# Kernel optimization log

Hardware: AMD Instinct MI355X
Metric: run time of the kernel (lower is better)

Reference implementation:

```python
import jax, jax.numpy as jnp
import numpy as np

N_NODES = 100000
N_EDGES = 1600000
D_IN = 128
LAYER_SIZES = [128, 128, 64]


def setup_inputs() -> dict:
    key = jax.random.key(0)
    ks = jax.random.split(key, 12)
    x = jax.random.normal(ks[0], (N_NODES, D_IN), dtype=jnp.float32)
    edge_index = jax.random.randint(ks[1], (2, N_EDGES), 0, N_NODES, dtype=jnp.int64)
    edge_weight = jax.random.uniform(ks[2], (N_EDGES,), dtype=jnp.float32)
    inp = {"x": x, "edge_index": edge_index, "edge_weight": edge_weight}
    dims = [D_IN] + LAYER_SIZES
    for i in range(len(LAYER_SIZES)):
        fan_in, fan_out = dims[i], dims[i + 1]
        # glorot-style init like PyG GCNConv
        scale = jnp.sqrt(6.0 / (fan_in + fan_out)).astype(jnp.float32)
        inp[f"W{i}"] = jax.random.uniform(ks[3 + 2 * i], (fan_in, fan_out), dtype=jnp.float32, minval=-scale, maxval=scale)
        inp[f"b{i}"] = jnp.zeros((fan_out,), dtype=jnp.float32)
    return inp


def _gcn_norm(edge_index, edge_weight, num_nodes):
    # PyG gcn_norm with add_self_loops=True (fill value 1.0)
    src, dst = edge_index[0], edge_index[1]
    loop = jnp.arange(num_nodes, dtype=edge_index.dtype)
    src_full = jnp.concatenate([src, loop])
    dst_full = jnp.concatenate([dst, loop])
    w_full = jnp.concatenate([edge_weight, jnp.ones((num_nodes,), dtype=edge_weight.dtype)])
    deg = jax.ops.segment_sum(w_full, dst_full, num_segments=num_nodes)  # [N]
    deg_inv_sqrt = jnp.where(deg > 0, jax.lax.rsqrt(jnp.where(deg > 0, deg, 1.0)), 0.0)
    norm = deg_inv_sqrt[src_full] * w_full * deg_inv_sqrt[dst_full]  # [E+N]
    return src_full, dst_full, norm


def _gcn_conv(x, src, dst, norm, W, b):
    h = x @ W                                  # [N, d_out] dense transform
    msg = h[src] * norm[:, None]               # [E+N, d_out] gather + scale
    out = jax.ops.segment_sum(msg, dst, num_segments=x.shape[0])  # scatter-add
    return out + b


def reference(x, edge_index, edge_weight, W0, b0, W1, b1, W2, b2):
    N = x.shape[0]
    src, dst, norm = _gcn_norm(edge_index, edge_weight, N)
    x = jax.nn.relu(_gcn_conv(x, src, dst, norm, W0, b0))
    x = jax.nn.relu(_gcn_conv(x, src, dst, norm, W1, b1))
    x = _gcn_conv(x, src, dst, norm, W2, b2)  # no ReLU on final layer
    return x
```

## Files before the change

kernel.cpp:

```cpp
#include <hip/hip_runtime.h>
#include <hip/hip_fp16.h>


typedef __attribute__((ext_vector_type(8))) _Float16 f16x8;
typedef __attribute__((ext_vector_type(4))) float f32x4;

#define WQ_BITS 15
#define WQ_SCALE 32768.0f
#define WQ_MASK 32767u

__global__ __launch_bounds__(256) void k_init(int* cnt, int N) {
    int i = blockIdx.x * 256 + threadIdx.x;
    if (i < N) cnt[i] = 0;
}

__global__ __launch_bounds__(256) void k_wprep(const float* __restrict__ W0,
                                               const float* __restrict__ W1,
                                               const float* __restrict__ W2,
                                               __half* __restrict__ wt0,
                                               __half* __restrict__ wt1,
                                               __half* __restrict__ wt2) {
    int id = blockIdx.x * 256 + threadIdx.x;
    if (id < 16384) {
        int n = id >> 7, k = id & 127;
        wt0[id] = __float2half(W0[k * 128 + n]);
    } else if (id < 32768) {
        int j = id - 16384, n = j >> 7, k = j & 127;
        wt1[j] = __float2half(W1[k * 128 + n]);
    } else if (id < 40960) {
        int j = id - 32768, n = j >> 7, k = j & 127;
        wt2[j] = __float2half(W2[k * 64 + n]);
    }
}

__global__ __launch_bounds__(256) void k_build(const int* __restrict__ src,
                                               const int* __restrict__ dst,
                                               const float* __restrict__ w,
                                               int* cnt, unsigned int* __restrict__ EW,
                                               int E, int cap) {
    int e = blockIdx.x * 256 + threadIdx.x;
    if (e >= E) return;
    int s = src[e], t = dst[e];
    int wq = (int)(w[e] * WQ_SCALE + 0.5f);
    wq = (wq < (int)WQ_MASK) ? wq : (int)WQ_MASK;
    int k = atomicAdd(&cnt[t], 1);
    if (k < cap) EW[(size_t)t * cap + k] = ((unsigned int)s << WQ_BITS) | (unsigned int)wq;
}

__global__ __launch_bounds__(256) void k_dinv(const int* __restrict__ cnt,
                                              const unsigned int* __restrict__ EW,
                                              float* __restrict__ dinv, int N, int cap) {
    int node = blockIdx.x * 4 + (threadIdx.x >> 6);
    if (node >= N) return;
    int lane = threadIdx.x & 63;
    int c = cnt[node];
    c = (c < cap) ? c : cap;
    float w = 0.f;
    if (lane < c) w = (float)(EW[(size_t)node * cap + lane] & WQ_MASK);
#pragma unroll
    for (int o = 32; o > 0; o >>= 1) w += __shfl_xor(w, o, 64);
    if (lane == 0) {
        float deg = 1.0f + w * (1.0f / WQ_SCALE);
        dinv[node] = 1.0f / sqrtf(deg);
    }
}

template <int BN, bool XFP32>
__global__ __launch_bounds__(256, 4) void k_gemm(const void* __restrict__ Xv,
                                                 const __half* __restrict__ Wt,
                                                 const float* __restrict__ dinv,
                                                 __half* __restrict__ H, int N) {
    constexpr int NT = BN / 16;
    const int lane = threadIdx.x & 63;
    const int wv = threadIdx.x >> 6;
    const int m = lane & 15;
    const int quad = lane >> 4;
    const int row = blockIdx.x * 64 + wv * 16 + m;
    const int rowc = (row < N) ? row : (N - 1);

    f16x8 xf[4];
    if constexpr (XFP32) {
        const float* X = (const float*)Xv;
#pragma unroll
        for (int s = 0; s < 4; s++) {
            const float4* p = (const float4*)(X + (size_t)rowc * 128 + s * 32 + quad * 8);
            float4 u0 = p[0], u1 = p[1];
            f16x8 f;
            f[0] = (_Float16)u0.x; f[1] = (_Float16)u0.y;
            f[2] = (_Float16)u0.z; f[3] = (_Float16)u0.w;
            f[4] = (_Float16)u1.x; f[5] = (_Float16)u1.y;
            f[6] = (_Float16)u1.z; f[7] = (_Float16)u1.w;
            xf[s] = f;
        }
    } else {
        const __half* X = (const __half*)Xv;
#pragma unroll
        for (int s = 0; s < 4; s++)
            xf[s] = *(const f16x8*)(X + (size_t)rowc * 128 + s * 32 + quad * 8);
    }

    f32x4 acc[NT];
#pragma unroll
    for (int t = 0; t < NT; t++) acc[t] = (f32x4){0.f, 0.f, 0.f, 0.f};

#pragma unroll
    for (int s = 0; s < 4; s++) {
#pragma unroll
        for (int t = 0; t < NT; t++) {
            f16x8 wf = *(const f16x8*)(Wt + (size_t)(t * 16 + m) * 128 + s * 32 + quad * 8);
            acc[t] = __builtin_amdgcn_mfma_f32_16x16x32_f16(wf, xf[s], acc[t], 0, 0, 0);
        }
    }

    if (row < N) {
        float sc = dinv[row];
#pragma unroll
        for (int t = 0; t < NT; t++) {
            __half2 h0 = __floats2half2_rn(sc * acc[t][0], sc * acc[t][1]);
            __half2 h1 = __floats2half2_rn(sc * acc[t][2], sc * acc[t][3]);
            __half2* dstp = (__half2*)(H + (size_t)row * BN + t * 16 + quad * 4);
            dstp[0] = h0;
            dstp[1] = h1;
        }
    }
}

#define RL(v, k) __builtin_amdgcn_readlane((v), (k))

template <int DOUT, bool RELU>
__global__ __launch_bounds__(256) void k_agg(const __half* __restrict__ H,
                                             const unsigned int* __restrict__ EW,
                                             const int* __restrict__ cnt,
                                             const float* __restrict__ dinv,
                                             const float* __restrict__ bias,
                                             void* __restrict__ Outv,
                                             int N, int cap) {
    int node = blockIdx.x * 4 + (threadIdx.x >> 6);
    if (node >= N) return;
    const int lane = threadIdx.x & 63;

    int c = cnt[node];
    c = (c < cap) ? c : cap;

    unsigned int meta = 0;
    if (lane < c) meta = EW[(size_t)node * cap + lane];

    float dt = dinv[node];

    if constexpr (DOUT == 128) {
        const __half2* H2 = reinterpret_cast<const __half2*>(H);
        float2 hs = __half22float2(H2[(size_t)node * 64 + lane]);
        float a0 = hs.x, a1 = hs.y;
        int k = 0;
        for (; k + 8 <= c; k += 8) {
            __half2 hr[8]; float w[8];
#pragma unroll
            for (int u = 0; u < 8; u++) {
                unsigned int mm = RL(meta, k + u);
                w[u] = (float)(mm & WQ_MASK) * (1.0f / WQ_SCALE);
                hr[u] = H2[(size_t)(mm >> WQ_BITS) * 64 + lane];
            }
#pragma unroll
            for (int u = 0; u < 8; u++) {
                float2 hv = __half22float2(hr[u]);
                a0 = fmaf(w[u], hv.x, a0);
                a1 = fmaf(w[u], hv.y, a1);
            }
        }
        for (; k + 4 <= c; k += 4) {
            __half2 hr[4]; float w[4];
#pragma unroll
            for (int u = 0; u < 4; u++) {
                unsigned int mm = RL(meta, k + u);
                w[u] = (float)(mm & WQ_MASK) * (1.0f / WQ_SCALE);
                hr[u] = H2[(size_t)(mm >> WQ_BITS) * 64 + lane];
            }
#pragma unroll
            for (int u = 0; u < 4; u++) {
                float2 hv = __half22float2(hr[u]);
                a0 = fmaf(w[u], hv.x, a0);
                a1 = fmaf(w[u], hv.y, a1);
            }
        }
        for (; k < c; k++) {
            unsigned int mm = RL(meta, k);
            float w = (float)(mm & WQ_MASK) * (1.0f / WQ_SCALE);
            float2 hv = __half22float2(H2[(size_t)(mm >> WQ_BITS) * 64 + lane]);
            a0 = fmaf(w, hv.x, a0);
            a1 = fmaf(w, hv.y, a1);
        }
        float2 b = reinterpret_cast<const float2*>(bias)[lane];
        a0 = fmaf(dt, a0, b.x);
        a1 = fmaf(dt, a1, b.y);
        if (RELU) { a0 = fmaxf(a0, 0.f); a1 = fmaxf(a1, 0.f); }
        reinterpret_cast<__half2*>(Outv)[(size_t)node * 64 + lane] = __floats2half2_rn(a0, a1);
    } else {
        float a = __half2float(H[(size_t)node * 64 + lane]);
        int k = 0;
        for (; k + 8 <= c; k += 8) {
            __half hr[8]; float w[8];
#pragma unroll
            for (int u = 0; u < 8; u++) {
                unsigned int mm = RL(meta, k + u);
                w[u] = (float)(mm & WQ_MASK) * (1.0f / WQ_SCALE);
                hr[u] = H[(size_t)(mm >> WQ_BITS) * 64 + lane];
            }
#pragma unroll
            for (int u = 0; u < 8; u++) a = fmaf(w[u], __half2float(hr[u]), a);
        }
        for (; k < c; k++) {
            unsigned int mm = RL(meta, k);
            float w = (float)(mm & WQ_MASK) * (1.0f / WQ_SCALE);
            a = fmaf(w, __half2float(H[(size_t)(mm >> WQ_BITS) * 64 + lane]), a);
        }
        a = fmaf(dt, a, bias[lane]);
        if (RELU) a = fmaxf(a, 0.f);
        ((float*)Outv)[(size_t)node * 64 + lane] = a;
    }
}

extern "C" void kernel_launch(void* const* d_in, const int* in_sizes, int n_in,
                              void* d_out, int out_size, void* d_ws, size_t ws_size,
                              hipStream_t stream) {
    const int N = in_sizes[0] / 128;
    const int E = in_sizes[2];

    const float* x  = (const float*)d_in[0];
    const int*   ei = (const int*)d_in[1];
    const int*   src = ei;
    const int*   dst = ei + E;
    const float* ew  = (const float*)d_in[2];
    const float* W0 = (const float*)d_in[3];
    const float* b0 = (const float*)d_in[4];
    const float* W1 = (const float*)d_in[5];
    const float* b1 = (const float*)d_in[6];
    const float* W2 = (const float*)d_in[7];
    const float* b2 = (const float*)d_in[8];

    size_t fixed = (((size_t)N * 4 + 255) & ~(size_t)255)
                 + (((size_t)N * 4 + 255) & ~(size_t)255)
                 + 2 * (((size_t)N * 128 * 2 + 255) & ~(size_t)255)
                 + 3 * 33024
                 + 2048;
    int cap = 64;
    if (ws_size > fixed) {
        size_t avail = (ws_size - fixed) / ((size_t)N * 4);
        if (avail < (size_t)cap) cap = (int)avail;
    } else {
        cap = 0;
    }

    char* p = (char*)d_ws;
    auto alloc = [&](size_t bytes) -> void* {
        void* r = (void*)p;
        p += (bytes + 255) & ~(size_t)255;
        return r;
    };
    int*          cnt  = (int*)alloc((size_t)N * 4);
    float*        dinv = (float*)alloc((size_t)N * 4);
    unsigned int* EW   = (unsigned int*)alloc((size_t)N * cap * 4);
    __half*       bufH = (__half*)alloc((size_t)N * 128 * 2);
    __half*       bufA = (__half*)alloc((size_t)N * 128 * 2);
    __half*       wt0  = (__half*)alloc(16384 * 2);
    __half*       wt1  = (__half*)alloc(16384 * 2);
    __half*       wt2  = (__half*)alloc(8192 * 2);

    dim3 blk(256);
    dim3 gN((N + 255) / 256), gE((E + 255) / 256);
    dim3 gGemm((N + 63) / 64);
    dim3 gWave((N + 3) / 4);

    k_init<<<gN, blk, 0, stream>>>(cnt, N);
    k_wprep<<<160, blk, 0, stream>>>(W0, W1, W2, wt0, wt1, wt2);
    k_build<<<gE, blk, 0, stream>>>(src, dst, ew, cnt, EW, E, cap);
    k_dinv<<<gWave, blk, 0, stream>>>(cnt, EW, dinv, N, cap);

    k_gemm<128, true><<<gGemm, blk, 0, stream>>>(x, wt0, dinv, bufH, N);
    k_agg<128, true><<<gWave, blk, 0, stream>>>(bufH, EW, cnt, dinv, b0, bufA, N, cap);

    k_gemm<128, false><<<gGemm, blk, 0, stream>>>(bufA, wt1, dinv, bufH, N);
    k_agg<128, true><<<gWave, blk, 0, stream>>>(bufH, EW, cnt, dinv, b1, bufA, N, cap);

    k_gemm<64, false><<<gGemm, blk, 0, stream>>>(bufA, wt2, dinv, bufH, N);
    k_agg<64, false><<<gWave, blk, 0, stream>>>(bufH, EW, cnt, dinv, b2,
                                                d_out, N, cap);
}
```

Baseline: 483.7 us.

## Fuse init/wprep, partition build atomics by dst group, fold dinv into first GEMM

Merges the counter-zeroing and weight-prep kernels into one launch, and folds the degree/dinv computation into the first GEMM kernel, which now computes dinv per block into shared memory and also writes it out. The edge-build kernel now uses a fixed grid where each block handles only edges whose destination falls in one of 8 partitions (by (t>>4)&7). The goal is to localize atomic traffic and CSR writes per partition, likely for better cache/XCD locality. In exchange, every edge is read 8 times for the filter check, and the GEMM gains a serial per-row degree loop before its MFMA work.

Result: faster. 448.2 us (-7.4%).

```diff
diff --git a/kernel.cpp b/kernel.cpp
--- a/kernel.cpp
+++ b/kernel.cpp
@@ -9,18 +9,15 @@
 #define WQ_SCALE 32768.0f
 #define WQ_MASK 32767u
 
-__global__ __launch_bounds__(256) void k_init(int* cnt, int N) {
-    int i = blockIdx.x * 256 + threadIdx.x;
-    if (i < N) cnt[i] = 0;
-}
-
-__global__ __launch_bounds__(256) void k_wprep(const float* __restrict__ W0,
-                                               const float* __restrict__ W1,
-                                               const float* __restrict__ W2,
-                                               __half* __restrict__ wt0,
-                                               __half* __restrict__ wt1,
-                                               __half* __restrict__ wt2) {
+__global__ __launch_bounds__(256) void k_pre(int* cnt, int N,
+                                             const float* __restrict__ W0,
+                                             const float* __restrict__ W1,
+                                             const float* __restrict__ W2,
+                                             __half* __restrict__ wt0,
+                                             __half* __restrict__ wt1,
+                                             __half* __restrict__ wt2) {
     int id = blockIdx.x * 256 + threadIdx.x;
+    if (id < N) cnt[id] = 0;
     if (id < 16384) {
         int n = id >> 7, k = id & 127;
         wt0[id] = __float2half(W0[k * 128 + n]);
@@ -38,45 +35,58 @@
                                                const float* __restrict__ w,
                                                int* cnt, unsigned int* __restrict__ EW,
                                                int E, int cap) {
-    int e = blockIdx.x * 256 + threadIdx.x;
-    if (e >= E) return;
-    int s = src[e], t = dst[e];
-    int wq = (int)(w[e] * WQ_SCALE + 0.5f);
-    wq = (wq < (int)WQ_MASK) ? wq : (int)WQ_MASK;
-    int k = atomicAdd(&cnt[t], 1);
-    if (k < cap) EW[(size_t)t * cap + k] = ((unsigned int)s << WQ_BITS) | (unsigned int)wq;
-}
-
-__global__ __launch_bounds__(256) void k_dinv(const int* __restrict__ cnt,
-                                              const unsigned int* __restrict__ EW,
-                                              float* __restrict__ dinv, int N, int cap) {
-    int node = blockIdx.x * 4 + (threadIdx.x >> 6);
-    if (node >= N) return;
-    int lane = threadIdx.x & 63;
-    int c = cnt[node];
-    c = (c < cap) ? c : cap;
-    float w = 0.f;
-    if (lane < c) w = (float)(EW[(size_t)node * cap + lane] & WQ_MASK);
-#pragma unroll
-    for (int o = 32; o > 0; o >>= 1) w += __shfl_xor(w, o, 64);
-    if (lane == 0) {
-        float deg = 1.0f + w * (1.0f / WQ_SCALE);
-        dinv[node] = 1.0f / sqrtf(deg);
-    }
-}
-
-template <int BN, bool XFP32>
+    const int p = blockIdx.x & 7;
+    const int chunk = blockIdx.x >> 3;
+    const int nchunk = gridDim.x >> 3;
+    const int stride = nchunk * 256;
+    for (int e = chunk * 256 + threadIdx.x; e < E; e += stride) {
+        int t = dst[e];
+        if (((t >> 4) & 7) != p) continue;
+        int s = src[e];
+        int wq = (int)(w[e] * WQ_SCALE + 0.5f);
+        wq = (wq < (int)WQ_MASK) ? wq : (int)WQ_MASK;
+        int k = atomicAdd(&cnt[t], 1);
+        if (k < cap) EW[(size_t)t * cap + k] = ((unsigned int)s << WQ_BITS) | (unsigned int)wq;
+    }
+}
+
+template <int BN, bool XFP32, bool DINV>
 __global__ __launch_bounds__(256, 4) void k_gemm(const void* __restrict__ Xv,
                                                  const __half* __restrict__ Wt,
-                                                 const float* __restrict__ dinv,
+                                                 float* __restrict__ dinv,
+                                                 const int* __restrict__ cnt,
+                                                 const unsigned int* __restrict__ EW,
+                                                 int cap,
                                                  __half* __restrict__ H, int N) {
-    constexpr int NT = BN / 16;
-    const int lane = threadIdx.x & 63;
-    const int wv = threadIdx.x >> 6;
+    __shared__ float dinv_s[64];
+    const int tid = threadIdx.x;
+    const int lane = tid & 63;
+    const int wv = tid >> 6;
     const int m = lane & 15;
     const int quad = lane >> 4;
-    const int row = blockIdx.x * 64 + wv * 16 + m;
+    const int rb = blockIdx.x * 64;
+    const int row = rb + wv * 16 + m;
     const int rowc = (row < N) ? row : (N - 1);
+
+    if constexpr (DINV) {
+        int rloc = tid >> 2, sub = tid & 3;
+        int r = rb + rloc;
+        float wsum = 0.f;
+        if (r < N) {
+            int c = cnt[r];
+            c = (c < cap) ? c : cap;
+            for (int j = sub; j < c; j += 4)
+                wsum += (float)(EW[(size_t)r * cap + j] & WQ_MASK);
+        }
+        wsum += __shfl_xor(wsum, 1, 64);
+        wsum += __shfl_xor(wsum, 2, 64);
+        float dv = 1.0f / sqrtf(1.0f + wsum * (1.0f / WQ_SCALE));
+        if (sub == 0) {
+            dinv_s[rloc] = dv;
+            if (r < N) dinv[r] = dv;
+        }
+        __syncthreads();
+    }
 
     f16x8 xf[4];
     if constexpr (XFP32) {
@@ -99,6 +109,7 @@
             xf[s] = *(const f16x8*)(X + (size_t)rowc * 128 + s * 32 + quad * 8);
     }
 
+    constexpr int NT = BN / 16;
     f32x4 acc[NT];
 #pragma unroll
     for (int t = 0; t < NT; t++) acc[t] = (f32x4){0.f, 0.f, 0.f, 0.f};
@@ -113,7 +124,7 @@
     }
 
     if (row < N) {
-        float sc = dinv[row];
+        float sc = DINV ? dinv_s[wv * 16 + m] : dinv[row];
 #pragma unroll
         for (int t = 0; t < NT; t++) {
             __half2 h0 = __floats2half2_rn(sc * acc[t][0], sc * acc[t][1]);
@@ -266,22 +277,22 @@
     __half*       wt2  = (__half*)alloc(8192 * 2);
 
     dim3 blk(256);
-    dim3 gN((N + 255) / 256), gE((E + 255) / 256);
+    int preN = (N > 40960) ? N : 40960;
+    dim3 gPre((preN + 255) / 256);
+    dim3 gBuild(6656);
     dim3 gGemm((N + 63) / 64);
     dim3 gWave((N + 3) / 4);
 
-    k_init<<<gN, blk, 0, stream>>>(cnt, N);
-    k_wprep<<<160, blk, 0, stream>>>(W0, W1, W2, wt0, wt1, wt2);
-    k_build<<<gE, blk, 0, stream>>>(src, dst, ew, cnt, EW, E, cap);
-    k_dinv<<<gWave, blk, 0, stream>>>(cnt, EW, dinv, N, cap);
-
-    k_gemm<128, true><<<gGemm, blk, 0, stream>>>(x, wt0, dinv, bufH, N);
+    k_pre<<<gPre, blk, 0, stream>>>(cnt, N, W0, W1, W2, wt0, wt1, wt2);
+    k_build<<<gBuild, blk, 0, stream>>>(src, dst, ew, cnt, EW, E, cap);
+
+    k_gemm<128, true, true><<<gGemm, blk, 0, stream>>>(x, wt0, dinv, cnt, EW, cap, bufH, N);
     k_agg<128, true><<<gWave, blk, 0, stream>>>(bufH, EW, cnt, dinv, b0, bufA, N, cap);
 
-    k_gemm<128, false><<<gGemm, blk, 0, stream>>>(bufA, wt1, dinv, bufH, N);
+    k_gemm<128, false, false><<<gGemm, blk, 0, stream>>>(bufA, wt1, dinv, cnt, EW, cap, bufH, N);
     k_agg<128, true><<<gWave, blk, 0, stream>>>(bufH, EW, cnt, dinv, b1, bufA, N, cap);
 
-    k_gemm<64, false><<<gGemm, blk, 0, stream>>>(bufA, wt2, dinv, bufH, N);
+    k_gemm<64, false, false><<<gGemm, blk, 0, stream>>>(bufA, wt2, dinv, cnt, EW, cap, bufH, N);
     k_agg<64, false><<<gWave, blk, 0, stream>>>(bufH, EW, cnt, dinv, b2,
                                                 d_out, N, cap);
 }
```
